# Kernel tuning notes

Hardware: AMD Instinct MI355X
Metric: run time of the kernel (lower is better)

Reference implementation:

```python
import jax, jax.numpy as jnp
import numpy as np
from jax import lax

B, H, E = 32, 2050, 128        # batch, input height, num_emb (conv width)
N = 2048                        # num_nodes = H - (kernel_size - 1)
C = 128                         # hidden_channels_CNN[0]
G1, G2 = 128, 128               # hidden_channels_GNN
MLP = 100                       # hidden_channels_MLP
OUT = 1                         # output_dim
KS = 3                          # kernel_size
NE = 32768                      # num edges


def setup_inputs() -> dict:
    key = jax.random.key(0)
    ks = jax.random.split(key, 12)
    s = 0.02
    inp = {
        "x": jax.random.normal(ks[0], (B, H, E), dtype=jnp.float32),
        "edge_index": jax.random.randint(ks[1], (2, NE), 0, N, dtype=jnp.int64),
        # Conv2d(1, C, kernel=(KS, E)) -> OIHW weight [C, 1, KS, E]
        "conv_w": jax.random.normal(ks[2], (C, 1, KS, E), dtype=jnp.float32) * s,
        "conv_b": jax.random.normal(ks[3], (C,), dtype=jnp.float32) * s,
        # GCNConv weights (linear has no bias; bias added after aggregation)
        "gW1": jax.random.normal(ks[4], (C, G1), dtype=jnp.float32) * s,
        "gb1": jax.random.normal(ks[5], (G1,), dtype=jnp.float32) * s,
        "gW2": jax.random.normal(ks[6], (G1, G2), dtype=jnp.float32) * s,
        "gb2": jax.random.normal(ks[7], (G2,), dtype=jnp.float32) * s,
        "W1": jax.random.normal(ks[8], (G2 * N, MLP), dtype=jnp.float32) * s,
        "b1": jax.random.normal(ks[9], (MLP,), dtype=jnp.float32) * s,
        "W2": jax.random.normal(ks[10], (MLP, OUT), dtype=jnp.float32) * s,
        "b2": jax.random.normal(ks[11], (OUT,), dtype=jnp.float32) * s,
    }
    return inp


def _gcn_norm(edge_index, n):
    # PyG gcn_norm with add_self_loops=True, edge_weight = 1
    loops = jnp.arange(n, dtype=edge_index.dtype)
    src = jnp.concatenate([edge_index[0], loops])
    dst = jnp.concatenate([edge_index[1], loops])
    deg = jax.ops.segment_sum(jnp.ones_like(dst, dtype=jnp.float32), dst, num_segments=n)
    dinv = jnp.where(deg > 0, lax.rsqrt(jnp.maximum(deg, 1.0)), 0.0)
    norm = dinv[src] * dinv[dst]
    return src, dst, norm


def _gcn_layer(h, src, dst, norm, W, b):
    # h: [B, N, Fin] -> out[b, dst] = sum_e norm_e * (h @ W)[b, src_e] + b
    hw = h @ W                                   # [B, N, Fout]
    msgs = hw[:, src, :] * norm[None, :, None]    # [B, E+N, Fout]
    agg = jnp.zeros_like(hw).at[:, dst, :].add(msgs)
    return agg + b


def reference(x, edge_index, conv_w, conv_b, gW1, gb1, gW2, gb2, W1, b1, W2, b2):
    # CNN feature extraction: [B,1,H,E] conv (KS,E) -> [B,C,N,1]
    x4 = x[:, None, :, :]
    h = lax.conv_general_dilated(x4, conv_w, window_strides=(1, 1), padding='VALID',
                                 dimension_numbers=('NCHW', 'OIHW', 'NCHW'))
    h = jax.nn.relu(h + conv_b[None, :, None, None])
    h = jnp.transpose(h[:, :, :, 0], (0, 2, 1))   # [B, N, C]

    src, dst, norm = _gcn_norm(edge_index, N)
    h = jax.nn.relu(_gcn_layer(h, src, dst, norm, gW1, gb1))
    h = jax.nn.relu(_gcn_layer(h, src, dst, norm, gW2, gb2))

    h = h.reshape(B, -1)                          # [B, N*G2]
    h = jax.nn.relu(h @ W1 + b1)
    # dropout: eval mode (identity)
    out = h @ W2 + b2
    return out.astype(jnp.float32)
```

## Files before the change

### kernel.cpp

```cpp
#include <hip/hip_runtime.h>
#include <stdint.h>

typedef unsigned short u16;
typedef __attribute__((ext_vector_type(8))) short bf16x8;
typedef __attribute__((ext_vector_type(4))) float f32x4;

#define NN 2048
#define NEDGE 32768
#define NBLK 1024
#define KC 256
#define NRG 4
#define PW 112

__device__ __forceinline__ float bf2f(uint32_t u) {
  union { uint32_t i; float f; } c; c.i = u << 16; return c.f;
}
__device__ __forceinline__ uint32_t f2bf(float f) {
  union { float f; uint32_t i; } c; c.f = f;
  uint32_t x = c.i;
  return (x + 0x7fffu + ((x >> 16) & 1u)) >> 16;
}

__global__ void k_cvt4(const float4* __restrict__ in, uint2* __restrict__ out, int n4) {
  int stride = gridDim.x * blockDim.x;
  for (int i = blockIdx.x * blockDim.x + threadIdx.x; i < n4; i += stride) {
    float4 v = in[i];
    uint2 o;
    o.x = f2bf(v.x) | (f2bf(v.y) << 16);
    o.y = f2bf(v.z) | (f2bf(v.w) << 16);
    out[i] = o;
  }
}

__global__ void k_prepw(const float4* __restrict__ cw, uint2* __restrict__ wtb,
                        const float* __restrict__ g1, const float* __restrict__ g2,
                        u16* __restrict__ o1, u16* __restrict__ o2) {
  int blk = blockIdx.x;
  if (blk < 48) {
    int i = blk * 256 + threadIdx.x;
    float4 v = cw[i];
    uint2 o;
    o.x = f2bf(v.x) | (f2bf(v.y) << 16);
    o.y = f2bf(v.z) | (f2bf(v.w) << 16);
    wtb[i] = o;
  } else {
    int i = (blk - 48) * 256 + threadIdx.x;
    int r = i >> 7, c = i & 127;
    o1[i] = (u16)f2bf(g1[c * 128 + r]);
    o2[i] = (u16)f2bf(g2[c * 128 + r]);
  }
}

__global__ void k_init(int* cnt, int* cursor) {
  int i = blockIdx.x * 256 + threadIdx.x;
  if (i < NN) { cnt[i] = 1; cursor[i] = 0; }
}

__global__ void k_count(const int* __restrict__ edge, int* __restrict__ cnt) {
  int i = blockIdx.x * 256 + threadIdx.x;
  if (i < NEDGE) atomicAdd(&cnt[edge[NEDGE + i]], 1);
}

__global__ __launch_bounds__(1024) void k_scan(const int* __restrict__ cnt, int* __restrict__ rowp) {
  __shared__ int s[1024];
  int t = threadIdx.x;
  int c0 = cnt[2 * t], c1 = cnt[2 * t + 1];
  s[t] = c0 + c1;
  __syncthreads();
  for (int off = 1; off < 1024; off <<= 1) {
    int v = (t >= off) ? s[t - off] : 0;
    __syncthreads();
    s[t] += v;
    __syncthreads();
  }
  int excl = s[t] - c0 - c1;
  rowp[2 * t] = excl;
  rowp[2 * t + 1] = excl + c0;
  if (t == 1023) rowp[2048] = s[t];
}

__global__ void k_fill(const int* __restrict__ edge, const int* __restrict__ cnt,
                       const int* __restrict__ rowp, int* __restrict__ cursor,
                       int* __restrict__ colx, float* __restrict__ wgt) {
  int i = blockIdx.x * 256 + threadIdx.x;
  if (i >= NEDGE + NN) return;
  int s, d;
  if (i < NEDGE) { s = edge[i]; d = edge[NEDGE + i]; }
  else { s = i - NEDGE; d = s; }
  float wv = rsqrtf((float)cnt[s] * (float)cnt[d]);
  int pos = atomicAdd(&cursor[d], 1);
  int idx = rowp[d] + pos;
  colx[idx] = s;
  wgt[idx] = wv;
}

__global__ __launch_bounds__(256) void k_gemm(
    const u16* __restrict__ A, const u16* __restrict__ Bt,
    const float* __restrict__ bias, u16* __restrict__ C,
    int K, int bExtra)
{
  __shared__ u16 lA[128 * 64];
  __shared__ u16 lB[128 * 64];
  const int t = threadIdx.x;
  const int Mbase = blockIdx.x * 128;
  const size_t aBase = (size_t)Mbase * 128 + (size_t)(Mbase >> 11) * bExtra;
  const int w = t >> 6, l = t & 63;
  const int wrM = (w >> 1) * 64, wrN = (w & 1) * 64;
  const int lm = l & 15, lkh = l >> 4;
  const int rph0 = t >> 3;
  const int pc = t & 7;
  f32x4 acc[4][4];
#pragma unroll
  for (int i = 0; i < 4; ++i)
#pragma unroll
    for (int j = 0; j < 4; ++j)
      acc[i][j] = (f32x4){0.f, 0.f, 0.f, 0.f};

  for (int kc = 0; kc < K; kc += 64) {
    __syncthreads();
#pragma unroll
    for (int it = 0; it < 4; ++it) {
      int r = it * 32 + rph0;
      int lc = pc ^ (r & 7);
      char* dstA = (char*)lA + it * 4096 + w * 1024;
      char* dstB = (char*)lB + it * 4096 + w * 1024;
      __builtin_amdgcn_global_load_lds(
          (const void*)(A + aBase + (size_t)r * 128 + kc + lc * 8), dstA, 16, 0, 0);
      __builtin_amdgcn_global_load_lds(
          (const void*)(Bt + (size_t)r * K + kc + lc * 8), dstB, 16, 0, 0);
    }
    __syncthreads();
#pragma unroll
    for (int kk = 0; kk < 2; ++kk) {
      int lc = kk * 4 + lkh;
      bf16x8 af[4], bfr[4];
#pragma unroll
      for (int i = 0; i < 4; ++i) {
        int R = wrM + i * 16 + lm;
        af[i] = *(const bf16x8*)((const char*)lA + R * 128 + ((lc ^ (R & 7)) << 4));
      }
#pragma unroll
      for (int j = 0; j < 4; ++j) {
        int R = wrN + j * 16 + lm;
        bfr[j] = *(const bf16x8*)((const char*)lB + R * 128 + ((lc ^ (R & 7)) << 4));
      }
#pragma unroll
      for (int i = 0; i < 4; ++i)
#pragma unroll
        for (int j = 0; j < 4; ++j)
          acc[i][j] = __builtin_amdgcn_mfma_f32_16x16x32_bf16(af[i], bfr[j], acc[i][j], 0, 0, 0);
    }
  }
  const int rq = (l >> 4) * 4;
#pragma unroll
  for (int i = 0; i < 4; ++i) {
#pragma unroll
    for (int j = 0; j < 4; ++j) {
      int col = wrN + j * 16 + lm;
      float bv = bias[col];
#pragma unroll
      for (int q = 0; q < 4; ++q) {
        int row = Mbase + wrM + i * 16 + rq + q;
        float v = acc[i][j][q] + bv;
        v = fmaxf(v, 0.f);
        C[(size_t)row * 128 + col] = (u16)f2bf(v);
      }
    }
  }
}

__global__ __launch_bounds__(256) void k_gather(
    const u16* __restrict__ h, const int* __restrict__ rowp,
    const int* __restrict__ colx, const float* __restrict__ wgt,
    u16* __restrict__ out)
{
  int w = threadIdx.x >> 6, l = threadIdx.x & 63;
  int p = blockIdx.x * 4 + w;
  int b = p >> 11, v = p & 2047;
  int e0 = rowp[v], e1 = rowp[v + 1];
  const u16* hb = h + (size_t)b * (2048 * 128);
  float a0 = 0.f, a1 = 0.f;
  int e = e0;
  for (; e + 4 <= e1; e += 4) {
    int u0 = colx[e], u1 = colx[e + 1], u2 = colx[e + 2], u3 = colx[e + 3];
    float w0 = wgt[e], w1 = wgt[e + 1], w2 = wgt[e + 2], w3 = wgt[e + 3];
    uint32_t k0 = *(const uint32_t*)(hb + (size_t)u0 * 128 + l * 2);
    uint32_t k1 = *(const uint32_t*)(hb + (size_t)u1 * 128 + l * 2);
    uint32_t k2 = *(const uint32_t*)(hb + (size_t)u2 * 128 + l * 2);
    uint32_t k3 = *(const uint32_t*)(hb + (size_t)u3 * 128 + l * 2);
    a0 += w0 * bf2f(k0 & 0xffffu) + w1 * bf2f(k1 & 0xffffu)
        + w2 * bf2f(k2 & 0xffffu) + w3 * bf2f(k3 & 0xffffu);
    a1 += w0 * bf2f(k0 >> 16) + w1 * bf2f(k1 >> 16)
        + w2 * bf2f(k2 >> 16) + w3 * bf2f(k3 >> 16);
  }
  for (; e < e1; ++e) {
    int u = colx[e];
    float wv = wgt[e];
    uint32_t pk = *(const uint32_t*)(hb + (size_t)u * 128 + l * 2);
    a0 += wv * bf2f(pk & 0xffffu);
    a1 += wv * bf2f(pk >> 16);
  }
  uint32_t o = f2bf(a0) | (f2bf(a1) << 16);
  *(uint32_t*)(out + (size_t)p * 128 + l * 2) = o;
}

__global__ __launch_bounds__(256) void k_mlp1(
    const u16* __restrict__ h3, const float* __restrict__ W1, float* __restrict__ part)
{
  __shared__ u16 sA[32][264];
  __shared__ u16 sB[112][264];
  const int t = threadIdx.x;
  const int blk = blockIdx.x;
  const int j0 = blk * KC;
  {
    int r = t >> 3, c = (t & 7) * 32;
    const u16* src = h3 + (size_t)r * 262144 + j0 + c;
#pragma unroll
    for (int u = 0; u < 4; ++u)
      *(bf16x8*)&sA[r][c + u * 8] = *(const bf16x8*)(src + u * 8);
  }
  for (int it = 0; it < 13; ++it) {
    int task = it * 256 + t;
    if (task < 3200) {
      int jp = task / 25, mq = task % 25;
      const float* wp = W1 + (size_t)(j0 + 2 * jp) * 100 + mq * 4;
      float4 fa = *(const float4*)wp;
      float4 fb = *(const float4*)(wp + 100);
      uint32_t p0 = f2bf(fa.x) | (f2bf(fb.x) << 16);
      uint32_t p1 = f2bf(fa.y) | (f2bf(fb.y) << 16);
      uint32_t p2 = f2bf(fa.z) | (f2bf(fb.z) << 16);
      uint32_t p3 = f2bf(fa.w) | (f2bf(fb.w) << 16);
      int m = mq * 4;
      *(uint32_t*)&sB[m + 0][2 * jp] = p0;
      *(uint32_t*)&sB[m + 1][2 * jp] = p1;
      *(uint32_t*)&sB[m + 2][2 * jp] = p2;
      *(uint32_t*)&sB[m + 3][2 * jp] = p3;
    }
  }
  __syncthreads();
  const int w = t >> 6, l = t & 63;
  const int mt = w >> 1, nh = w & 1;
  const int nt0 = nh * 4, ntn = nh ? 3 : 4;
  const int lm = l & 15, lk8 = (l >> 4) * 8;
  f32x4 acc[4];
#pragma unroll
  for (int n = 0; n < 4; ++n) acc[n] = (f32x4){0.f, 0.f, 0.f, 0.f};
#pragma unroll
  for (int kk = 0; kk < 8; ++kk) {
    int ko = kk * 32 + lk8;
    bf16x8 af = *(const bf16x8*)&sA[mt * 16 + lm][ko];
#pragma unroll
    for (int n = 0; n < 4; ++n) {
      if (n < ntn) {
        bf16x8 bfr = *(const bf16x8*)&sB[(nt0 + n) * 16 + lm][ko];
        acc[n] = __builtin_amdgcn_mfma_f32_16x16x32_bf16(af, bfr, acc[n], 0, 0, 0);
      }
    }
  }
  const int rq = (l >> 4) * 4;
#pragma unroll
  for (int n = 0; n < 4; ++n) {
    if (n < ntn) {
      int m = (nt0 + n) * 16 + lm;
#pragma unroll
      for (int q = 0; q < 4; ++q) {
        int b = mt * 16 + rq + q;
        part[((size_t)blk * 32 + b) * PW + m] = acc[n][q];
      }
    }
  }
}

__global__ __launch_bounds__(256) void k_red(
    const float* __restrict__ part, float* __restrict__ part2)
{
  int e = blockIdx.x * 256 + threadIdx.x;
  int rg = blockIdx.y;
  const float* p = part + (size_t)rg * 256 * (32 * PW) + e;
  float s0 = 0.f, s1 = 0.f, s2 = 0.f, s3 = 0.f;
  for (int r = 0; r < 256; r += 4) {
    s0 += p[(size_t)(r + 0) * (32 * PW)];
    s1 += p[(size_t)(r + 1) * (32 * PW)];
    s2 += p[(size_t)(r + 2) * (32 * PW)];
    s3 += p[(size_t)(r + 3) * (32 * PW)];
  }
  part2[rg * (32 * PW) + e] = (s0 + s1) + (s2 + s3);
}

__global__ __launch_bounds__(128) void k_mlp2(
    const float* __restrict__ part2, const float* __restrict__ b1,
    const float* __restrict__ W2, const float* __restrict__ b2, float* __restrict__ out)
{
  __shared__ float sh[100];
  int b = blockIdx.x, t = threadIdx.x;
  if (t < 100) {
    float s = 0.f;
#pragma unroll
    for (int rg = 0; rg < NRG; ++rg)
      s += part2[rg * (32 * PW) + b * PW + t];
    float h = fmaxf(s + b1[t], 0.f);
    sh[t] = h * W2[t];
  }
  __syncthreads();
  if (t == 0) {
    float s = 0.f;
    for (int m = 0; m < 100; ++m) s += sh[m];
    out[b] = s + b2[0];
  }
}

extern "C" void kernel_launch(void* const* d_in, const int* in_sizes, int n_in,
                              void* d_out, int out_size, void* d_ws, size_t ws_size,
                              hipStream_t stream) {
  (void)in_sizes; (void)n_in; (void)out_size; (void)ws_size;
  const float* x      = (const float*)d_in[0];
  const int* edge     = (const int*)d_in[1];
  const float* conv_w = (const float*)d_in[2];
  const float* conv_b = (const float*)d_in[3];
  const float* gW1    = (const float*)d_in[4];
  const float* gb1    = (const float*)d_in[5];
  const float* gW2    = (const float*)d_in[6];
  const float* gb2    = (const float*)d_in[7];
  const float* W1     = (const float*)d_in[8];
  const float* b1     = (const float*)d_in[9];
  const float* W2     = (const float*)d_in[10];
  const float* b2     = (const float*)d_in[11];
  float* out = (float*)d_out;

  char* ws = (char*)d_ws;
  size_t off = 0;
  auto alloc = [&](size_t bytes) {
    void* p = ws + off;
    off = (off + bytes + 255) & ~(size_t)255;
    return p;
  };
  u16* xb     = (u16*)alloc(8396800ull * 2);
  u16* bufA   = (u16*)alloc(8388608ull * 2);
  u16* bufB   = (u16*)alloc(8388608ull * 2);
  u16* Wtb    = (u16*)alloc(49152ull * 2);
  u16* g1t    = (u16*)alloc(16384ull * 2);
  u16* g2t    = (u16*)alloc(16384ull * 2);
  int* cnt    = (int*)alloc(2048 * 4);
  int* cursor = (int*)alloc(2048 * 4);
  int* rowp   = (int*)alloc(2052 * 4);
  int* colx   = (int*)alloc(34816 * 4);
  float* wgt  = (float*)alloc(34816 * 4);
  float* part2= (float*)alloc((size_t)NRG * (32 * PW) * 4);
  float* part = (float*)xb;

  k_init<<<8, 256, 0, stream>>>(cnt, cursor);
  k_count<<<128, 256, 0, stream>>>(edge, cnt);
  k_scan<<<1, 1024, 0, stream>>>(cnt, rowp);
  k_fill<<<(NEDGE + NN + 255) / 256, 256, 0, stream>>>(edge, cnt, rowp, cursor, colx, wgt);

  k_cvt4<<<2048, 256, 0, stream>>>((const float4*)x, (uint2*)xb, 8396800 / 4);
  k_prepw<<<112, 256, 0, stream>>>((const float4*)conv_w, (uint2*)Wtb, gW1, gW2, g1t, g2t);

  k_gemm<<<512, 256, 0, stream>>>(xb, Wtb, conv_b, bufA, 384, 256);
  k_gather<<<16384, 256, 0, stream>>>(bufA, rowp, colx, wgt, bufB);
  k_gemm<<<512, 256, 0, stream>>>(bufB, g1t, gb1, bufA, 128, 0);
  k_gather<<<16384, 256, 0, stream>>>(bufA, rowp, colx, wgt, bufB);
  k_gemm<<<512, 256, 0, stream>>>(bufB, g2t, gb2, bufA, 128, 0);
  k_mlp1<<<NBLK, 256, 0, stream>>>(bufA, W1, part);
  k_red<<<dim3(14, NRG), 256, 0, stream>>>(part, part2);
  k_mlp2<<<32, 128, 0, stream>>>(part2, b1, W2, b2, out);
}
```

Measured before the change: 203.4 us.

## Fuse GCN aggregation with weight GEMM and merge prep kernels

```diff
diff --git a/kernel.cpp b/kernel.cpp
--- a/kernel.cpp
+++ b/kernel.cpp
@@ -21,30 +21,29 @@
   return (x + 0x7fffu + ((x >> 16) & 1u)) >> 16;
 }
 
-__global__ void k_cvt4(const float4* __restrict__ in, uint2* __restrict__ out, int n4) {
-  int stride = gridDim.x * blockDim.x;
-  for (int i = blockIdx.x * blockDim.x + threadIdx.x; i < n4; i += stride) {
-    float4 v = in[i];
-    uint2 o;
-    o.x = f2bf(v.x) | (f2bf(v.y) << 16);
-    o.y = f2bf(v.z) | (f2bf(v.w) << 16);
-    out[i] = o;
-  }
-}
-
-__global__ void k_prepw(const float4* __restrict__ cw, uint2* __restrict__ wtb,
-                        const float* __restrict__ g1, const float* __restrict__ g2,
-                        u16* __restrict__ o1, u16* __restrict__ o2) {
+__global__ void k_prep(const float4* __restrict__ x4, uint2* __restrict__ xb,
+                       const float4* __restrict__ cw, uint2* __restrict__ wtb,
+                       const float* __restrict__ g1, const float* __restrict__ g2,
+                       u16* __restrict__ o1, u16* __restrict__ o2) {
   int blk = blockIdx.x;
-  if (blk < 48) {
-    int i = blk * 256 + threadIdx.x;
+  if (blk < 2048) {
+    const int n4 = 8396800 / 4;
+    for (int i = blk * 256 + threadIdx.x; i < n4; i += 2048 * 256) {
+      float4 v = x4[i];
+      uint2 o;
+      o.x = f2bf(v.x) | (f2bf(v.y) << 16);
+      o.y = f2bf(v.z) | (f2bf(v.w) << 16);
+      xb[i] = o;
+    }
+  } else if (blk < 2096) {
+    int i = (blk - 2048) * 256 + threadIdx.x;
     float4 v = cw[i];
     uint2 o;
     o.x = f2bf(v.x) | (f2bf(v.y) << 16);
     o.y = f2bf(v.z) | (f2bf(v.w) << 16);
     wtb[i] = o;
   } else {
-    int i = (blk - 48) * 256 + threadIdx.x;
+    int i = (blk - 2096) * 256 + threadIdx.x;
     int r = i >> 7, c = i & 127;
     o1[i] = (u16)f2bf(g1[c * 128 + r]);
     o2[i] = (u16)f2bf(g2[c * 128 + r]);
@@ -169,39 +168,114 @@
   }
 }
 
-__global__ __launch_bounds__(256) void k_gather(
+__global__ __launch_bounds__(256) void k_gcn(
     const u16* __restrict__ h, const int* __restrict__ rowp,
     const int* __restrict__ colx, const float* __restrict__ wgt,
-    u16* __restrict__ out)
+    const u16* __restrict__ Bt, const float* __restrict__ bias,
+    u16* __restrict__ C)
 {
-  int w = threadIdx.x >> 6, l = threadIdx.x & 63;
-  int p = blockIdx.x * 4 + w;
-  int b = p >> 11, v = p & 2047;
-  int e0 = rowp[v], e1 = rowp[v + 1];
+  __shared__ u16 lA[64 * 128];
+  __shared__ u16 lB[128 * 128];
+  const int t = threadIdx.x;
+  const int w = t >> 6, l = t & 63;
+  const int Mbase = blockIdx.x * 64;
+  const int b = Mbase >> 11, v0 = Mbase & 2047;
   const u16* hb = h + (size_t)b * (2048 * 128);
-  float a0 = 0.f, a1 = 0.f;
-  int e = e0;
-  for (; e + 4 <= e1; e += 4) {
-    int u0 = colx[e], u1 = colx[e + 1], u2 = colx[e + 2], u3 = colx[e + 3];
-    float w0 = wgt[e], w1 = wgt[e + 1], w2 = wgt[e + 2], w3 = wgt[e + 3];
-    uint32_t k0 = *(const uint32_t*)(hb + (size_t)u0 * 128 + l * 2);
-    uint32_t k1 = *(const uint32_t*)(hb + (size_t)u1 * 128 + l * 2);
-    uint32_t k2 = *(const uint32_t*)(hb + (size_t)u2 * 128 + l * 2);
-    uint32_t k3 = *(const uint32_t*)(hb + (size_t)u3 * 128 + l * 2);
-    a0 += w0 * bf2f(k0 & 0xffffu) + w1 * bf2f(k1 & 0xffffu)
-        + w2 * bf2f(k2 & 0xffffu) + w3 * bf2f(k3 & 0xffffu);
-    a1 += w0 * bf2f(k0 >> 16) + w1 * bf2f(k1 >> 16)
-        + w2 * bf2f(k2 >> 16) + w3 * bf2f(k3 >> 16);
-  }
-  for (; e < e1; ++e) {
-    int u = colx[e];
-    float wv = wgt[e];
-    uint32_t pk = *(const uint32_t*)(hb + (size_t)u * 128 + l * 2);
-    a0 += wv * bf2f(pk & 0xffffu);
-    a1 += wv * bf2f(pk >> 16);
-  }
-  uint32_t o = f2bf(a0) | (f2bf(a1) << 16);
-  *(uint32_t*)(out + (size_t)p * 128 + l * 2) = o;
+
+  {
+    int r = t >> 1, half = t & 1;
+#pragma unroll
+    for (int u = 0; u < 8; ++u) {
+      int ch = half * 8 + u;
+      *(bf16x8*)((char*)lB + r * 256 + ((ch ^ (r & 15)) << 4)) =
+          *(const bf16x8*)(Bt + (size_t)r * 128 + ch * 8);
+    }
+  }
+
+  for (int rr = 0; rr < 16; ++rr) {
+    int r = w * 16 + rr;
+    int v = v0 + r;
+    int e0 = rowp[v], e1 = rowp[v + 1];
+    float a0 = 0.f, a1 = 0.f;
+    int e = e0;
+    for (; e + 8 <= e1; e += 8) {
+      int u0 = colx[e], u1 = colx[e + 1], u2 = colx[e + 2], u3 = colx[e + 3];
+      int u4 = colx[e + 4], u5 = colx[e + 5], u6 = colx[e + 6], u7 = colx[e + 7];
+      float w0 = wgt[e], w1 = wgt[e + 1], w2 = wgt[e + 2], w3 = wgt[e + 3];
+      float w4 = wgt[e + 4], w5 = wgt[e + 5], w6 = wgt[e + 6], w7 = wgt[e + 7];
+      uint32_t k0 = *(const uint32_t*)(hb + (size_t)u0 * 128 + l * 2);
+      uint32_t k1 = *(const uint32_t*)(hb + (size_t)u1 * 128 + l * 2);
+      uint32_t k2 = *(const uint32_t*)(hb + (size_t)u2 * 128 + l * 2);
+      uint32_t k3 = *(const uint32_t*)(hb + (size_t)u3 * 128 + l * 2);
+      uint32_t k4 = *(const uint32_t*)(hb + (size_t)u4 * 128 + l * 2);
+      uint32_t k5 = *(const uint32_t*)(hb + (size_t)u5 * 128 + l * 2);
+      uint32_t k6 = *(const uint32_t*)(hb + (size_t)u6 * 128 + l * 2);
+      uint32_t k7 = *(const uint32_t*)(hb + (size_t)u7 * 128 + l * 2);
+      a0 += w0 * bf2f(k0 & 0xffffu) + w1 * bf2f(k1 & 0xffffu)
+          + w2 * bf2f(k2 & 0xffffu) + w3 * bf2f(k3 & 0xffffu)
+          + w4 * bf2f(k4 & 0xffffu) + w5 * bf2f(k5 & 0xffffu)
+          + w6 * bf2f(k6 & 0xffffu) + w7 * bf2f(k7 & 0xffffu);
+      a1 += w0 * bf2f(k0 >> 16) + w1 * bf2f(k1 >> 16)
+          + w2 * bf2f(k2 >> 16) + w3 * bf2f(k3 >> 16)
+          + w4 * bf2f(k4 >> 16) + w5 * bf2f(k5 >> 16)
+          + w6 * bf2f(k6 >> 16) + w7 * bf2f(k7 >> 16);
+    }
+    for (; e < e1; ++e) {
+      int u = colx[e];
+      float wv = wgt[e];
+      uint32_t pk = *(const uint32_t*)(hb + (size_t)u * 128 + l * 2);
+      a0 += wv * bf2f(pk & 0xffffu);
+      a1 += wv * bf2f(pk >> 16);
+    }
+    uint32_t o = f2bf(a0) | (f2bf(a1) << 16);
+    *(uint32_t*)((char*)lA + r * 256 + (((l >> 2) ^ (r & 15)) << 4) + (l & 3) * 4) = o;
+  }
+  __syncthreads();
+
+  const int wrM = (w >> 1) * 32, wrN = (w & 1) * 64;
+  const int lm = l & 15, kg = l >> 4;
+  f32x4 acc[2][4];
+#pragma unroll
+  for (int i = 0; i < 2; ++i)
+#pragma unroll
+    for (int j = 0; j < 4; ++j)
+      acc[i][j] = (f32x4){0.f, 0.f, 0.f, 0.f};
+#pragma unroll
+  for (int kk = 0; kk < 4; ++kk) {
+    int ck = kk * 4 + kg;
+    bf16x8 af[2], bfr[4];
+#pragma unroll
+    for (int i = 0; i < 2; ++i) {
+      int R = wrM + i * 16 + lm;
+      af[i] = *(const bf16x8*)((const char*)lA + R * 256 + ((ck ^ (R & 15)) << 4));
+    }
+#pragma unroll
+    for (int j = 0; j < 4; ++j) {
+      int R = wrN + j * 16 + lm;
+      bfr[j] = *(const bf16x8*)((const char*)lB + R * 256 + ((ck ^ (R & 15)) << 4));
+    }
+#pragma unroll
+    for (int i = 0; i < 2; ++i)
+#pragma unroll
+      for (int j = 0; j < 4; ++j)
+        acc[i][j] = __builtin_amdgcn_mfma_f32_16x16x32_bf16(af[i], bfr[j], acc[i][j], 0, 0, 0);
+  }
+  const int rq = (l >> 4) * 4;
+#pragma unroll
+  for (int i = 0; i < 2; ++i) {
+#pragma unroll
+    for (int j = 0; j < 4; ++j) {
+      int col = wrN + j * 16 + lm;
+      float bv = bias[col];
+#pragma unroll
+      for (int q = 0; q < 4; ++q) {
+        int row = Mbase + wrM + i * 16 + rq + q;
+        float v = acc[i][j][q] + bv;
+        v = fmaxf(v, 0.f);
+        C[(size_t)row * 128 + col] = (u16)f2bf(v);
+      }
+    }
+  }
 }
 
 __global__ __launch_bounds__(256) void k_mlp1(
@@ -353,14 +427,13 @@
   k_scan<<<1, 1024, 0, stream>>>(cnt, rowp);
   k_fill<<<(NEDGE + NN + 255) / 256, 256, 0, stream>>>(edge, cnt, rowp, cursor, colx, wgt);
 
-  k_cvt4<<<2048, 256, 0, stream>>>((const float4*)x, (uint2*)xb, 8396800 / 4);
-  k_prepw<<<112, 256, 0, stream>>>((const float4*)conv_w, (uint2*)Wtb, gW1, gW2, g1t, g2t);
+  k_prep<<<2160, 256, 0, stream>>>((const float4*)x, (uint2*)xb,
+                                   (const float4*)conv_w, (uint2*)Wtb,
+                                   gW1, gW2, g1t, g2t);
 
   k_gemm<<<512, 256, 0, stream>>>(xb, Wtb, conv_b, bufA, 384, 256);
-  k_gather<<<16384, 256, 0, stream>>>(bufA, rowp, colx, wgt, bufB);
-  k_gemm<<<512, 256, 0, stream>>>(bufB, g1t, gb1, bufA, 128, 0);
-  k_gather<<<16384, 256, 0, stream>>>(bufA, rowp, colx, wgt, bufB);
-  k_gemm<<<512, 256, 0, stream>>>(bufB, g2t, gb2, bufA, 128, 0);
+  k_gcn<<<1024, 256, 0, stream>>>(bufA, rowp, colx, wgt, g1t, gb1, bufB);
+  k_gcn<<<1024, 256, 0, stream>>>(bufB, rowp, colx, wgt, g2t, gb2, bufA);
   k_mlp1<<<NBLK, 256, 0, stream>>>(bufA, W1, part);
   k_red<<<dim3(14, NRG), 256, 0, stream>>>(part, part2);
   k_mlp2<<<32, 128, 0, stream>>>(part2, b1, W2, b2, out);
```

Measured after the change: 326.3 us. +60.4%, slower.
